# Kernel optimization log

Hardware: AMD Instinct MI355X
Metric: run time of the kernel (lower is better)

Reference implementation:

```python
import jax, jax.numpy as jnp
import numpy as np

N, E, T, H, D_IN, D_OUT = 50000, 320000, 4, 4, 128, 128
NEG_SLOPE = 0.2
LN_EPS = 1e-5


def setup_inputs() -> dict:
    key = jax.random.key(0)
    ks = jax.random.split(key, 10)
    x = jax.random.normal(ks[0], (N, D_IN), jnp.float32)
    edge_index = jax.random.randint(ks[1], (2, E), 0, N, jnp.int32)
    edge_attr = jax.random.randint(ks[2], (E,), 0, T, jnp.int32)
    W_gat = jax.random.normal(ks[3], (T, D_IN, H * D_OUT), jnp.float32) / np.sqrt(D_IN)
    a_src = jax.random.normal(ks[4], (T, H, D_OUT), jnp.float32) / np.sqrt(D_OUT)
    a_dst = jax.random.normal(ks[5], (T, H, D_OUT), jnp.float32) / np.sqrt(D_OUT)
    b_gat = jnp.zeros((T, D_OUT), jnp.float32)
    edge_type_weights = jnp.ones((T,), jnp.float32) / T
    W_fuse = jax.random.normal(ks[6], (T * D_OUT, D_OUT), jnp.float32) / np.sqrt(T * D_OUT)
    b_fuse = jnp.zeros((D_OUT,), jnp.float32)
    ln_gamma = jnp.ones((D_OUT,), jnp.float32)
    ln_beta = jnp.zeros((D_OUT,), jnp.float32)
    return {"x": x, "edge_index": edge_index, "edge_attr": edge_attr,
            "W_gat": W_gat, "a_src": a_src, "a_dst": a_dst, "b_gat": b_gat,
            "edge_type_weights": edge_type_weights, "W_fuse": W_fuse,
            "b_fuse": b_fuse, "ln_gamma": ln_gamma, "ln_beta": ln_beta}


def _gat_one_type(x, src_all, dst_all, mask_all, W, a_s, a_d, b):
    # x: [N, D_in]; src_all/dst_all: [E+N] (type-mask + self-loops on all nodes)
    n = x.shape[0]
    h = (x @ W).reshape(n, H, D_OUT)                      # [N, H, D]
    alpha_s = jnp.sum(h * a_s, axis=-1)                   # [N, H]
    alpha_d = jnp.sum(h * a_d, axis=-1)                   # [N, H]
    logit = jax.nn.leaky_relu(alpha_s[src_all] + alpha_d[dst_all], NEG_SLOPE)  # [Ea, H]
    neg_inf = jnp.float32(-1e30)
    logit = jnp.where(mask_all[:, None], logit, neg_inf)
    m = jax.ops.segment_max(logit, dst_all, num_segments=n)   # [N, H] (self-loops ensure finite)
    ex = jnp.exp(logit - m[dst_all])
    ex = jnp.where(mask_all[:, None], ex, 0.0)
    denom = jax.ops.segment_sum(ex, dst_all, num_segments=n)  # [N, H]
    alpha = ex / denom[dst_all]                                # [Ea, H]
    msg = alpha[:, :, None] * h[src_all]                       # [Ea, H, D]
    out = jax.ops.segment_sum(msg, dst_all, num_segments=n)   # [N, H, D]
    return out.mean(axis=1) + b                                # concat=False -> head mean


def reference(x, edge_index, edge_attr, W_gat, a_src, a_dst, b_gat,
              edge_type_weights, W_fuse, b_fuse, ln_gamma, ln_beta):
    n = x.shape[0]
    self_idx = jnp.arange(n, dtype=edge_index.dtype)
    src_all = jnp.concatenate([edge_index[0], self_idx])
    dst_all = jnp.concatenate([edge_index[1], self_idx])
    outs = []
    for t in range(T):
        mask_all = jnp.concatenate([edge_attr == t, jnp.ones((n,), bool)])
        outs.append(_gat_one_type(x, src_all, dst_all, mask_all,
                                  W_gat[t], a_src[t], a_dst[t], b_gat[t]))
    w = jax.nn.softmax(edge_type_weights)
    x_cat = jnp.concatenate([outs[t] * w[t] for t in range(T)], axis=1)  # [N, T*D]
    y = x_cat @ W_fuse + b_fuse
    mu = jnp.mean(y, axis=-1, keepdims=True)
    var = jnp.var(y, axis=-1, keepdims=True)
    y = (y - mu) / jnp.sqrt(var + LN_EPS) * ln_gamma + ln_beta
    return jax.nn.relu(y)
```

## Files before the change

### kernel.cpp

```cpp
#include <hip/hip_runtime.h>
#include <hip/hip_bf16.h>

#define TT 4
#define HH 4
#define DD 128
#define KAGG 2048

typedef __attribute__((ext_vector_type(8))) short short8;
typedef __attribute__((ext_vector_type(4))) float f32x4;

__device__ __forceinline__ float lrelu(float z) { return z > 0.f ? z : 0.2f * z; }
__device__ __forceinline__ float bf2f(unsigned short u) {
  union { unsigned int i; float f; } v; v.i = ((unsigned int)u) << 16; return v.f;
}
__device__ __forceinline__ unsigned short f2b(float f) {
  union { float f; unsigned int i; } u; u.f = f;
  unsigned int r = u.i + 0x7fff + ((u.i >> 16) & 1);
  return (unsigned short)(r >> 16);
}
__device__ __forceinline__ void unpack8(uint4 u, float* hv) {
  hv[0] = bf2f((unsigned short)(u.x & 0xffff));
  hv[1] = bf2f((unsigned short)(u.x >> 16));
  hv[2] = bf2f((unsigned short)(u.y & 0xffff));
  hv[3] = bf2f((unsigned short)(u.y >> 16));
  hv[4] = bf2f((unsigned short)(u.z & 0xffff));
  hv[5] = bf2f((unsigned short)(u.z >> 16));
  hv[6] = bf2f((unsigned short)(u.w & 0xffff));
  hv[7] = bf2f((unsigned short)(u.w >> 16));
}

__global__ __launch_bounds__(256) void convx_kernel(
    const float* __restrict__ x, unsigned short* __restrict__ xb, int total4) {
  int i = blockIdx.x * 256 + threadIdx.x;
  if (i >= total4) return;
  float4 v = ((const float4*)x)[i];
  ushort4 o;
  o.x = f2b(v.x); o.y = f2b(v.y); o.z = f2b(v.z); o.w = f2b(v.w);
  ((ushort4*)xb)[i] = o;
}

__global__ __launch_bounds__(256) void prepw_kernel(
    const float* __restrict__ Wg, const float* __restrict__ a_s,
    const float* __restrict__ a_d, const float* __restrict__ W_fuse,
    const float* __restrict__ b_gat, const float* __restrict__ etw,
    const float* __restrict__ b_fuse, unsigned short* __restrict__ Gfrag,
    unsigned short* __restrict__ Pall, float* __restrict__ cbias) {
  float e0 = etw[0], e1 = etw[1], e2 = etw[2], e3 = etw[3];
  float mx = fmaxf(fmaxf(e0, e1), fmaxf(e2, e3));
  float w0 = __expf(e0 - mx), w1 = __expf(e1 - mx), w2 = __expf(e2 - mx),
        w3 = __expf(e3 - mx);
  float inv = 1.f / (w0 + w1 + w2 + w3);
  float wts[4] = {w0 * inv, w1 * inv, w2 * inv, w3 * inv};

  int bid = blockIdx.x;
  if (bid < 1024) {
    int idx = bid * 256 + threadIdx.x;
    int f = idx >> 9, l = (idx >> 3) & 63, j = idx & 7;
    int kt = f >> 5, kk = (f >> 3) & 3, n = f & 7;
    int K = kt * 128 + kk * 32 + (l >> 4) * 8 + j;
    int col = n * 16 + (l & 15);
    int t = K >> 9, head = (K >> 7) & 3, k = K & 127;
    const float* wr = Wg + (size_t)t * 65536 + k * 512 + head * 128;
    const float* wf = W_fuse + (size_t)t * 128 * 128 + col;
    float s = 0.f;
    for (int m = 0; m < 128; ++m) s += wr[m] * wf[(size_t)m * 128];
    Gfrag[idx] = f2b(0.25f * wts[t] * s);
  } else if (bid < 1040) {
    int idx = (bid - 1024) * 256 + threadIdx.x;
    int c = idx >> 7, k = idx & 127;
    int t = c >> 3, jj = c & 7, head = jj & 3;
    const float* av = ((jj < 4) ? a_s : a_d) + (t * 4 + head) * 128;
    const float* wr = Wg + (size_t)t * 65536 + k * 512 + head * 128;
    float s = 0.f;
    for (int m = 0; m < 128; ++m) s += wr[m] * av[m];
    Pall[c * 128 + k] = f2b(s);
  } else {
    int j = threadIdx.x;
    if (j < 128) {
      float s = b_fuse[j];
      for (int t = 0; t < 4; ++t) {
        float st = 0.f;
        for (int m = 0; m < 128; ++m)
          st += b_gat[t * 128 + m] * W_fuse[(size_t)(t * 128 + m) * 128 + j];
        s += wts[t] * st;
      }
      cbias[j] = s;
    }
  }
}

__global__ __launch_bounds__(256) void alpha_mfma_kernel(
    const unsigned short* __restrict__ xb, const unsigned short* __restrict__ Pall,
    float* __restrict__ as_, float* __restrict__ ad_, int N) {
  __shared__ uint4 ldsv[2048];
  unsigned char* lds = (unsigned char*)ldsv;
  const int n0 = blockIdx.x * 128;
  const int tid = threadIdx.x, lane = tid & 63, wid = tid >> 6;
  const int lr = lane & 15, lg = lane >> 4;
#pragma unroll
  for (int i = 0; i < 8; ++i) {
    int chunk = tid + i * 256;
    int row = chunk >> 4, k16 = chunk & 15;
    int gr = n0 + row;
    uint4 v = make_uint4(0, 0, 0, 0);
    if (gr < N) v = *(const uint4*)(xb + (size_t)gr * DD + k16 * 8);
    *(uint4*)(lds + ((row * 256 + k16 * 16) ^ ((row & 7) << 4))) = v;
  }
  __syncthreads();
  f32x4 acc[2][2] = {};
#pragma unroll
  for (int kk = 0; kk < 4; ++kk) {
    short8 a[2], b[2];
#pragma unroll
    for (int m = 0; m < 2; ++m) {
      int row = wid * 32 + m * 16 + lr;
      a[m] = *(const short8*)(lds + ((row * 256 + kk * 64 + (lg << 4)) ^ ((row & 7) << 4)));
    }
#pragma unroll
    for (int n = 0; n < 2; ++n) {
      int c = n * 16 + lr;
      b[n] = *(const short8*)(Pall + c * DD + kk * 32 + lg * 8);
    }
#pragma unroll
    for (int m = 0; m < 2; ++m)
#pragma unroll
      for (int n = 0; n < 2; ++n)
        acc[m][n] = __builtin_amdgcn_mfma_f32_16x16x32_bf16(a[m], b[n], acc[m][n], 0, 0, 0);
  }
#pragma unroll
  for (int m = 0; m < 2; ++m)
#pragma unroll
    for (int n = 0; n < 2; ++n) {
      int c = n * 16 + lr;
      int t = c >> 3, jj = c & 7, head = jj & 3;
      float* dstp = (jj & 4) ? ad_ : as_;
#pragma unroll
      for (int r = 0; r < 4; ++r) {
        int gr = n0 + wid * 32 + m * 16 + lg * 4 + r;
        if (gr < N) dstp[((size_t)t * N + gr) * 4 + head] = acc[m][n][r];
      }
    }
}

__global__ __launch_bounds__(256) void hist_kernel(
    const int* __restrict__ dst, const int* __restrict__ attr,
    int* __restrict__ deg, int E, int N) {
  int e = blockIdx.x * 256 + threadIdx.x;
  if (e < E) atomicAdd(&deg[attr[e] * N + dst[e]], 1);
}

__global__ __launch_bounds__(1024) void scan1_kernel(
    const int* __restrict__ deg, int* __restrict__ rowptr,
    int* __restrict__ sums, int M) {
  __shared__ int sh[1024];
  int i = blockIdx.x * 1024 + threadIdx.x;
  int v = (i < M) ? deg[i] : 0;
  sh[threadIdx.x] = v;
  __syncthreads();
  for (int off = 1; off < 1024; off <<= 1) {
    int x = (threadIdx.x >= off) ? sh[threadIdx.x - off] : 0;
    __syncthreads();
    sh[threadIdx.x] += x;
    __syncthreads();
  }
  if (i < M) rowptr[i] = sh[threadIdx.x] - v;
  if (threadIdx.x == 1023) sums[blockIdx.x] = sh[1023];
}

__global__ __launch_bounds__(256) void scan2_kernel(int* __restrict__ sums, int nch) {
  __shared__ int sh[256];
  int v = (threadIdx.x < nch) ? sums[threadIdx.x] : 0;
  sh[threadIdx.x] = v;
  __syncthreads();
  for (int off = 1; off < 256; off <<= 1) {
    int x = (threadIdx.x >= off) ? sh[threadIdx.x - off] : 0;
    __syncthreads();
    sh[threadIdx.x] += x;
    __syncthreads();
  }
  if (threadIdx.x < nch) sums[threadIdx.x] = sh[threadIdx.x] - v;
}

__global__ __launch_bounds__(1024) void scan3_kernel(
    int* __restrict__ rowptr, const int* __restrict__ sums,
    int* __restrict__ cursor, int M) {
  int i = blockIdx.x * 1024 + threadIdx.x;
  if (i < M) {
    int r = rowptr[i] + sums[blockIdx.x];
    rowptr[i] = r;
    cursor[i] = r;
  }
}

__global__ __launch_bounds__(256) void scatter_kernel(
    const int* __restrict__ src, const int* __restrict__ dst,
    const int* __restrict__ attr, int* __restrict__ cursor,
    int* __restrict__ slist, int E, int N) {
  int e = blockIdx.x * 256 + threadIdx.x;
  if (e >= E) return;
  int p = atomicAdd(&cursor[attr[e] * N + dst[e]], 1);
  slist[p] = src[e];
}

__global__ __launch_bounds__(256) void gather_kernel(
    const int* __restrict__ slist, const int* __restrict__ rowptr,
    const int* __restrict__ deg, const float* __restrict__ as_,
    const float* __restrict__ ad_, const unsigned short* __restrict__ xb,
    unsigned short* __restrict__ AGG, int N) {
  int t = blockIdx.y;
  int d = blockIdx.x * 4 + (threadIdx.x >> 6);
  if (d >= N) return;
  int lane = threadIdx.x & 63;
  int head = lane >> 4;
  int dofs = (lane & 15) * 8;
  size_t tn = (size_t)t * N;

  float adh = ad_[(tn + d) * 4 + head];
  float es = __expf(lrelu(as_[(tn + d) * 4 + head] + adh));
  float den = es;
  float acc8[8], hv[8];
  unpack8(*(const uint4*)(xb + (size_t)d * DD + dofs), hv);
#pragma unroll
  for (int j = 0; j < 8; ++j) acc8[j] = es * hv[j];

  int base = rowptr[tn + d], dg = deg[tn + d];
  int i = 0;
  for (; i + 1 < dg; i += 2) {
    int s0 = slist[base + i], s1 = slist[base + i + 1];
    float av0 = as_[(tn + s0) * 4 + head];
    float av1 = as_[(tn + s1) * 4 + head];
    uint4 u0 = *(const uint4*)(xb + (size_t)s0 * DD + dofs);
    uint4 u1 = *(const uint4*)(xb + (size_t)s1 * DD + dofs);
    float q0 = __expf(lrelu(av0 + adh));
    float q1 = __expf(lrelu(av1 + adh));
    den += q0 + q1;
    unpack8(u0, hv);
#pragma unroll
    for (int j = 0; j < 8; ++j) acc8[j] += q0 * hv[j];
    unpack8(u1, hv);
#pragma unroll
    for (int j = 0; j < 8; ++j) acc8[j] += q1 * hv[j];
  }
  if (i < dg) {
    int s = slist[base + i];
    float av = as_[(tn + s) * 4 + head];
    uint4 u = *(const uint4*)(xb + (size_t)s * DD + dofs);
    float q = __expf(lrelu(av + adh));
    den += q;
    unpack8(u, hv);
#pragma unroll
    for (int j = 0; j < 8; ++j) acc8[j] += q * hv[j];
  }

  float r = 1.f / den;
  unsigned int p0 = (unsigned)f2b(acc8[0] * r) | ((unsigned)f2b(acc8[1] * r) << 16);
  unsigned int p1 = (unsigned)f2b(acc8[2] * r) | ((unsigned)f2b(acc8[3] * r) << 16);
  unsigned int p2 = (unsigned)f2b(acc8[4] * r) | ((unsigned)f2b(acc8[5] * r) << 16);
  unsigned int p3 = (unsigned)f2b(acc8[6] * r) | ((unsigned)f2b(acc8[7] * r) << 16);
  *(uint4*)(AGG + (size_t)d * KAGG + t * 512 + lane * 8) = make_uint4(p0, p1, p2, p3);
}

__global__ __launch_bounds__(256) void gemmln_kernel(
    const unsigned short* __restrict__ AGG, const unsigned short* __restrict__ Gfrag,
    const float* __restrict__ cbias, const float* __restrict__ gamma,
    const float* __restrict__ beta, float* __restrict__ out, int N) {
  __shared__ uint4 bbuf[2][2048];
  const int n0 = blockIdx.x * 128;
  const int tid = threadIdx.x, lane = tid & 63, wid = tid >> 6;
  const int lr = lane & 15, lg = lane >> 4;
  const int wrow = n0 + wid * 32;

  uint4 bn[8], an[8], ac[8];
#pragma unroll
  for (int i = 0; i < 8; ++i)
    bn[i] = *(const uint4*)(Gfrag + (size_t)(i * 256 + tid) * 8);
#pragma unroll
  for (int i = 0; i < 8; ++i) {
    int m = i >> 2, kk = i & 3;
    int gr = wrow + m * 16 + lr;
    an[i] = make_uint4(0, 0, 0, 0);
    if (gr < N) an[i] = *(const uint4*)(AGG + (size_t)gr * KAGG + kk * 32 + lg * 8);
  }
#pragma unroll
  for (int i = 0; i < 8; ++i) bbuf[0][i * 256 + tid] = bn[i];
  __syncthreads();
#pragma unroll
  for (int i = 0; i < 8; ++i) ac[i] = an[i];

  f32x4 acc[2][8] = {};
  int cur = 0;
  for (int kt = 0; kt < 16; ++kt) {
    if (kt < 15) {
#pragma unroll
      for (int i = 0; i < 8; ++i)
        bn[i] = *(const uint4*)(Gfrag + (size_t)(kt + 1) * 16384 + (size_t)(i * 256 + tid) * 8);
#pragma unroll
      for (int i = 0; i < 8; ++i) {
        int m = i >> 2, kk = i & 3;
        int gr = wrow + m * 16 + lr;
        an[i] = make_uint4(0, 0, 0, 0);
        if (gr < N)
          an[i] = *(const uint4*)(AGG + (size_t)gr * KAGG + (kt + 1) * 128 + kk * 32 + lg * 8);
      }
    }
    const unsigned char* lds = (const unsigned char*)bbuf[cur];
#pragma unroll
    for (int kk = 0; kk < 4; ++kk) {
      short8 a0 = *(const short8*)&ac[0 * 4 + kk];
      short8 a1 = *(const short8*)&ac[1 * 4 + kk];
#pragma unroll
      for (int n = 0; n < 8; ++n) {
        short8 b = *(const short8*)(lds + (kk * 8 + n) * 1024 + lane * 16);
        acc[0][n] = __builtin_amdgcn_mfma_f32_16x16x32_bf16(a0, b, acc[0][n], 0, 0, 0);
        acc[1][n] = __builtin_amdgcn_mfma_f32_16x16x32_bf16(a1, b, acc[1][n], 0, 0, 0);
      }
    }
    if (kt < 15) {
#pragma unroll
      for (int i = 0; i < 8; ++i) bbuf[cur ^ 1][i * 256 + tid] = bn[i];
      __syncthreads();
      cur ^= 1;
#pragma unroll
      for (int i = 0; i < 8; ++i) ac[i] = an[i];
    }
  }

  float cb[8], gm[8], bt[8];
#pragma unroll
  for (int n = 0; n < 8; ++n) {
    cb[n] = cbias[n * 16 + lr];
    gm[n] = gamma[n * 16 + lr];
    bt[n] = beta[n * 16 + lr];
  }
#pragma unroll
  for (int m = 0; m < 2; ++m)
#pragma unroll
    for (int rr = 0; rr < 4; ++rr) {
      float y[8];
      float s = 0.f, ss = 0.f;
#pragma unroll
      for (int n = 0; n < 8; ++n) {
        y[n] = acc[m][n][rr] + cb[n];
        s += y[n];
        ss += y[n] * y[n];
      }
#pragma unroll
      for (int mask = 1; mask <= 8; mask <<= 1) {
        s += __shfl_xor(s, mask);
        ss += __shfl_xor(ss, mask);
      }
      float mean = s * (1.f / 128.f);
      float var = ss * (1.f / 128.f) - mean * mean;
      float rstd = rsqrtf(var + 1e-5f);
      int gr = wrow + m * 16 + lg * 4 + rr;
      if (gr < N) {
#pragma unroll
        for (int n = 0; n < 8; ++n) {
          float v = (y[n] - mean) * rstd * gm[n] + bt[n];
          out[(size_t)gr * DD + n * 16 + lr] = fmaxf(0.f, v);
        }
      }
    }
}

extern "C" void kernel_launch(void* const* d_in, const int* in_sizes, int n_in,
                              void* d_out, int out_size, void* d_ws, size_t ws_size,
                              hipStream_t stream) {
  const float* x      = (const float*)d_in[0];
  const int*   ei     = (const int*)d_in[1];
  const int*   attr   = (const int*)d_in[2];
  const float* Wg     = (const float*)d_in[3];
  const float* a_src  = (const float*)d_in[4];
  const float* a_dst  = (const float*)d_in[5];
  const float* b_gat  = (const float*)d_in[6];
  const float* etw    = (const float*)d_in[7];
  const float* W_fuse = (const float*)d_in[8];
  const float* b_fuse = (const float*)d_in[9];
  const float* gamma  = (const float*)d_in[10];
  const float* beta   = (const float*)d_in[11];

  const int N = in_sizes[0] / DD;
  const int E = in_sizes[2];
  const int* src = ei;
  const int* dst = ei + E;
  const int M = TT * N;

  char* ws = (char*)d_ws;
  size_t off = 0;
  auto alloc = [&](size_t bytes) {
    void* p = ws + off;
    off += (bytes + 255) & ~(size_t)255;
    return p;
  };
  unsigned short* AGG   = (unsigned short*)alloc((size_t)N * KAGG * 2);
  unsigned short* xb    = (unsigned short*)alloc((size_t)N * DD * 2);
  unsigned short* Gfrag = (unsigned short*)alloc((size_t)512 * 512 * 2);
  unsigned short* Pall  = (unsigned short*)alloc((size_t)32 * DD * 2);
  float* cbias          = (float*)alloc(128 * sizeof(float));
  float* as_            = (float*)alloc((size_t)TT * N * 4 * sizeof(float));
  float* ad_            = (float*)alloc((size_t)TT * N * 4 * sizeof(float));
  int* deg              = (int*)alloc((size_t)M * sizeof(int));
  int* rowptr           = (int*)alloc((size_t)M * sizeof(int));
  int* cursor           = (int*)alloc((size_t)M * sizeof(int));
  int* slist            = (int*)alloc((size_t)E * sizeof(int));
  int* sums             = (int*)alloc(1024 * sizeof(int));

  hipMemsetAsync(deg, 0, (size_t)M * sizeof(int), stream);

  int total4x = N * DD / 4;
  convx_kernel<<<(total4x + 255) / 256, 256, 0, stream>>>(x, xb, total4x);
  prepw_kernel<<<1041, 256, 0, stream>>>(Wg, a_src, a_dst, W_fuse, b_gat, etw,
                                         b_fuse, Gfrag, Pall, cbias);
  hist_kernel<<<(E + 255) / 256, 256, 0, stream>>>(dst, attr, deg, E, N);
  int nch = (M + 1023) / 1024;
  scan1_kernel<<<nch, 1024, 0, stream>>>(deg, rowptr, sums, M);
  scan2_kernel<<<1, 256, 0, stream>>>(sums, nch);
  scan3_kernel<<<nch, 1024, 0, stream>>>(rowptr, sums, cursor, M);
  scatter_kernel<<<(E + 255) / 256, 256, 0, stream>>>(src, dst, attr, cursor, slist, E, N);

  alpha_mfma_kernel<<<(N + 127) / 128, 256, 0, stream>>>(xb, Pall, as_, ad_, N);

  dim3 ggrid((N + 3) / 4, TT);
  gather_kernel<<<ggrid, 256, 0, stream>>>(slist, rowptr, deg, as_, ad_, xb, AGG, N);

  gemmln_kernel<<<(N + 127) / 128, 256, 0, stream>>>(AGG, Gfrag, cbias, gamma, beta,
                                                     (float*)d_out, N);
}
```

Before: 209.9 us.

## Fuse prologue, scan and scatter/alpha kernels; shortcut empty rows; nontemporal AGG traffic

Merges the bf16 conversion, weight precompute and degree histogram into one launch. It replaces the three-pass scan with a single-pass scan that claims per-block bases through a global atomic counter, and fuses the CSR scatter with the alpha MFMA kernel. This cuts several launches and dependency gaps. The gather kernel now copies the node's own features directly when a (node, type) pair has no incoming edges, skipping the softmax work. AGG stores and loads use nontemporal hints to limit cache pollution. The atomic-based scan leaves segment order nondeterministic, but offsets stay disjoint.

```diff
diff --git a/kernel.cpp b/kernel.cpp
--- a/kernel.cpp
+++ b/kernel.cpp
@@ -8,6 +8,7 @@
 
 typedef __attribute__((ext_vector_type(8))) short short8;
 typedef __attribute__((ext_vector_type(4))) float f32x4;
+typedef __attribute__((ext_vector_type(4))) unsigned int uint4v;
 
 __device__ __forceinline__ float lrelu(float z) { return z > 0.f ? z : 0.2f * z; }
 __device__ __forceinline__ float bf2f(unsigned short u) {
@@ -18,7 +19,7 @@
   unsigned int r = u.i + 0x7fff + ((u.i >> 16) & 1);
   return (unsigned short)(r >> 16);
 }
-__device__ __forceinline__ void unpack8(uint4 u, float* hv) {
+__device__ __forceinline__ void unpack8v(uint4v u, float* hv) {
   hv[0] = bf2f((unsigned short)(u.x & 0xffff));
   hv[1] = bf2f((unsigned short)(u.x >> 16));
   hv[2] = bf2f((unsigned short)(u.y & 0xffff));
@@ -29,72 +30,120 @@
   hv[7] = bf2f((unsigned short)(u.w >> 16));
 }
 
-__global__ __launch_bounds__(256) void convx_kernel(
-    const float* __restrict__ x, unsigned short* __restrict__ xb, int total4) {
-  int i = blockIdx.x * 256 + threadIdx.x;
-  if (i >= total4) return;
-  float4 v = ((const float4*)x)[i];
-  ushort4 o;
-  o.x = f2b(v.x); o.y = f2b(v.y); o.z = f2b(v.z); o.w = f2b(v.w);
-  ((ushort4*)xb)[i] = o;
-}
-
-__global__ __launch_bounds__(256) void prepw_kernel(
+__global__ __launch_bounds__(256) void prologue_kernel(
+    const float* __restrict__ x, unsigned short* __restrict__ xb, int total4,
     const float* __restrict__ Wg, const float* __restrict__ a_s,
     const float* __restrict__ a_d, const float* __restrict__ W_fuse,
     const float* __restrict__ b_gat, const float* __restrict__ etw,
     const float* __restrict__ b_fuse, unsigned short* __restrict__ Gfrag,
-    unsigned short* __restrict__ Pall, float* __restrict__ cbias) {
-  float e0 = etw[0], e1 = etw[1], e2 = etw[2], e3 = etw[3];
-  float mx = fmaxf(fmaxf(e0, e1), fmaxf(e2, e3));
-  float w0 = __expf(e0 - mx), w1 = __expf(e1 - mx), w2 = __expf(e2 - mx),
-        w3 = __expf(e3 - mx);
-  float inv = 1.f / (w0 + w1 + w2 + w3);
-  float wts[4] = {w0 * inv, w1 * inv, w2 * inv, w3 * inv};
-
+    unsigned short* __restrict__ Pall, float* __restrict__ cbias,
+    const int* __restrict__ dst, const int* __restrict__ attr,
+    int* __restrict__ deg, int E, int N) {
   int bid = blockIdx.x;
-  if (bid < 1024) {
-    int idx = bid * 256 + threadIdx.x;
-    int f = idx >> 9, l = (idx >> 3) & 63, j = idx & 7;
-    int kt = f >> 5, kk = (f >> 3) & 3, n = f & 7;
-    int K = kt * 128 + kk * 32 + (l >> 4) * 8 + j;
-    int col = n * 16 + (l & 15);
-    int t = K >> 9, head = (K >> 7) & 3, k = K & 127;
-    const float* wr = Wg + (size_t)t * 65536 + k * 512 + head * 128;
-    const float* wf = W_fuse + (size_t)t * 128 * 128 + col;
-    float s = 0.f;
-    for (int m = 0; m < 128; ++m) s += wr[m] * wf[(size_t)m * 128];
-    Gfrag[idx] = f2b(0.25f * wts[t] * s);
-  } else if (bid < 1040) {
-    int idx = (bid - 1024) * 256 + threadIdx.x;
-    int c = idx >> 7, k = idx & 127;
-    int t = c >> 3, jj = c & 7, head = jj & 3;
-    const float* av = ((jj < 4) ? a_s : a_d) + (t * 4 + head) * 128;
-    const float* wr = Wg + (size_t)t * 65536 + k * 512 + head * 128;
-    float s = 0.f;
-    for (int m = 0; m < 128; ++m) s += wr[m] * av[m];
-    Pall[c * 128 + k] = f2b(s);
-  } else {
-    int j = threadIdx.x;
-    if (j < 128) {
-      float s = b_fuse[j];
-      for (int t = 0; t < 4; ++t) {
-        float st = 0.f;
-        for (int m = 0; m < 128; ++m)
-          st += b_gat[t * 128 + m] * W_fuse[(size_t)(t * 128 + m) * 128 + j];
-        s += wts[t] * st;
-      }
-      cbias[j] = s;
-    }
-  }
-}
-
-__global__ __launch_bounds__(256) void alpha_mfma_kernel(
-    const unsigned short* __restrict__ xb, const unsigned short* __restrict__ Pall,
-    float* __restrict__ as_, float* __restrict__ ad_, int N) {
+  const int nconv = (total4 + 255) >> 8;
+  if (bid < nconv) {
+    int i = bid * 256 + threadIdx.x;
+    if (i < total4) {
+      float4 v = ((const float4*)x)[i];
+      ushort4 o;
+      o.x = f2b(v.x); o.y = f2b(v.y); o.z = f2b(v.z); o.w = f2b(v.w);
+      ((ushort4*)xb)[i] = o;
+    }
+    return;
+  }
+  bid -= nconv;
+  if (bid < 1041) {
+    float e0 = etw[0], e1 = etw[1], e2 = etw[2], e3 = etw[3];
+    float mx = fmaxf(fmaxf(e0, e1), fmaxf(e2, e3));
+    float w0 = __expf(e0 - mx), w1 = __expf(e1 - mx), w2 = __expf(e2 - mx),
+          w3 = __expf(e3 - mx);
+    float inv = 1.f / (w0 + w1 + w2 + w3);
+    float wts[4] = {w0 * inv, w1 * inv, w2 * inv, w3 * inv};
+    if (bid < 1024) {
+      int idx = bid * 256 + threadIdx.x;
+      int f = idx >> 9, l = (idx >> 3) & 63, j = idx & 7;
+      int kt = f >> 5, kk = (f >> 3) & 3, n = f & 7;
+      int K = kt * 128 + kk * 32 + (l >> 4) * 8 + j;
+      int col = n * 16 + (l & 15);
+      int t = K >> 9, head = (K >> 7) & 3, k = K & 127;
+      const float* wr = Wg + (size_t)t * 65536 + k * 512 + head * 128;
+      const float* wf = W_fuse + (size_t)t * 128 * 128 + col;
+      float s = 0.f;
+      for (int m = 0; m < 128; ++m) s += wr[m] * wf[(size_t)m * 128];
+      Gfrag[idx] = f2b(0.25f * wts[t] * s);
+    } else if (bid < 1040) {
+      int idx = (bid - 1024) * 256 + threadIdx.x;
+      int c = idx >> 7, k = idx & 127;
+      int t = c >> 3, jj = c & 7, head = jj & 3;
+      const float* av = ((jj < 4) ? a_s : a_d) + (t * 4 + head) * 128;
+      const float* wr = Wg + (size_t)t * 65536 + k * 512 + head * 128;
+      float s = 0.f;
+      for (int m = 0; m < 128; ++m) s += wr[m] * av[m];
+      Pall[c * 128 + k] = f2b(s);
+    } else {
+      int j = threadIdx.x;
+      if (j < 128) {
+        float s = b_fuse[j];
+        for (int t = 0; t < 4; ++t) {
+          float st = 0.f;
+          for (int m = 0; m < 128; ++m)
+            st += b_gat[t * 128 + m] * W_fuse[(size_t)(t * 128 + m) * 128 + j];
+          s += wts[t] * st;
+        }
+        cbias[j] = s;
+      }
+    }
+    return;
+  }
+  bid -= 1041;
+  int e = bid * 256 + threadIdx.x;
+  if (e < E) atomicAdd(&deg[attr[e] * N + dst[e]], 1);
+}
+
+__global__ __launch_bounds__(1024) void scanfused_kernel(
+    const int* __restrict__ deg, int* __restrict__ rowptr,
+    int* __restrict__ cursor, int* __restrict__ gcur, int M) {
+  __shared__ int sh[1024];
+  __shared__ int base;
+  int i = blockIdx.x * 1024 + threadIdx.x;
+  int v = (i < M) ? deg[i] : 0;
+  sh[threadIdx.x] = v;
+  __syncthreads();
+  for (int off = 1; off < 1024; off <<= 1) {
+    int xx = (threadIdx.x >= off) ? sh[threadIdx.x - off] : 0;
+    __syncthreads();
+    sh[threadIdx.x] += xx;
+    __syncthreads();
+  }
+  if (threadIdx.x == 1023) base = atomicAdd(gcur, sh[1023]);
+  __syncthreads();
+  if (i < M) {
+    int r = base + sh[threadIdx.x] - v;
+    rowptr[i] = r;
+    cursor[i] = r;
+  }
+}
+
+__global__ __launch_bounds__(256) void scatter_alpha_kernel(
+    const int* __restrict__ src, const int* __restrict__ dst,
+    const int* __restrict__ attr, int* __restrict__ cursor,
+    int* __restrict__ slist, const unsigned short* __restrict__ xb,
+    const unsigned short* __restrict__ Pall, float* __restrict__ as_,
+    float* __restrict__ ad_, int E, int N) {
   __shared__ uint4 ldsv[2048];
+  int bid = blockIdx.x;
+  const int nsc = (E + 255) >> 8;
+  if (bid < nsc) {
+    int e = bid * 256 + threadIdx.x;
+    if (e < E) {
+      int p = atomicAdd(&cursor[attr[e] * N + dst[e]], 1);
+      slist[p] = src[e];
+    }
+    return;
+  }
+  bid -= nsc;
   unsigned char* lds = (unsigned char*)ldsv;
-  const int n0 = blockIdx.x * 128;
+  const int n0 = bid * 128;
   const int tid = threadIdx.x, lane = tid & 63, wid = tid >> 6;
   const int lr = lane & 15, lg = lane >> 4;
 #pragma unroll
@@ -140,66 +189,6 @@
         if (gr < N) dstp[((size_t)t * N + gr) * 4 + head] = acc[m][n][r];
       }
     }
-}
-
-__global__ __launch_bounds__(256) void hist_kernel(
-    const int* __restrict__ dst, const int* __restrict__ attr,
-    int* __restrict__ deg, int E, int N) {
-  int e = blockIdx.x * 256 + threadIdx.x;
-  if (e < E) atomicAdd(&deg[attr[e] * N + dst[e]], 1);
-}
-
-__global__ __launch_bounds__(1024) void scan1_kernel(
-    const int* __restrict__ deg, int* __restrict__ rowptr,
-    int* __restrict__ sums, int M) {
-  __shared__ int sh[1024];
-  int i = blockIdx.x * 1024 + threadIdx.x;
-  int v = (i < M) ? deg[i] : 0;
-  sh[threadIdx.x] = v;
-  __syncthreads();
-  for (int off = 1; off < 1024; off <<= 1) {
-    int x = (threadIdx.x >= off) ? sh[threadIdx.x - off] : 0;
-    __syncthreads();
-    sh[threadIdx.x] += x;
-    __syncthreads();
-  }
-  if (i < M) rowptr[i] = sh[threadIdx.x] - v;
-  if (threadIdx.x == 1023) sums[blockIdx.x] = sh[1023];
-}
-
-__global__ __launch_bounds__(256) void scan2_kernel(int* __restrict__ sums, int nch) {
-  __shared__ int sh[256];
-  int v = (threadIdx.x < nch) ? sums[threadIdx.x] : 0;
-  sh[threadIdx.x] = v;
-  __syncthreads();
-  for (int off = 1; off < 256; off <<= 1) {
-    int x = (threadIdx.x >= off) ? sh[threadIdx.x - off] : 0;
-    __syncthreads();
-    sh[threadIdx.x] += x;
-    __syncthreads();
-  }
-  if (threadIdx.x < nch) sums[threadIdx.x] = sh[threadIdx.x] - v;
-}
-
-__global__ __launch_bounds__(1024) void scan3_kernel(
-    int* __restrict__ rowptr, const int* __restrict__ sums,
-    int* __restrict__ cursor, int M) {
-  int i = blockIdx.x * 1024 + threadIdx.x;
-  if (i < M) {
-    int r = rowptr[i] + sums[blockIdx.x];
-    rowptr[i] = r;
-    cursor[i] = r;
-  }
-}
-
-__global__ __launch_bounds__(256) void scatter_kernel(
-    const int* __restrict__ src, const int* __restrict__ dst,
-    const int* __restrict__ attr, int* __restrict__ cursor,
-    int* __restrict__ slist, int E, int N) {
-  int e = blockIdx.x * 256 + threadIdx.x;
-  if (e >= E) return;
-  int p = atomicAdd(&cursor[attr[e] * N + dst[e]], 1);
-  slist[p] = src[e];
 }
 
 __global__ __launch_bounds__(256) void gather_kernel(
@@ -214,50 +203,58 @@
   int head = lane >> 4;
   int dofs = (lane & 15) * 8;
   size_t tn = (size_t)t * N;
+  uint4v* outp = (uint4v*)(AGG + (size_t)d * KAGG + t * 512 + lane * 8);
+
+  int base = rowptr[tn + d], dg = deg[tn + d];
+  if (dg == 0) {
+    uint4v u = *(const uint4v*)(xb + (size_t)d * DD + dofs);
+    __builtin_nontemporal_store(u, outp);
+    return;
+  }
 
   float adh = ad_[(tn + d) * 4 + head];
   float es = __expf(lrelu(as_[(tn + d) * 4 + head] + adh));
   float den = es;
   float acc8[8], hv[8];
-  unpack8(*(const uint4*)(xb + (size_t)d * DD + dofs), hv);
+  unpack8v(*(const uint4v*)(xb + (size_t)d * DD + dofs), hv);
 #pragma unroll
   for (int j = 0; j < 8; ++j) acc8[j] = es * hv[j];
 
-  int base = rowptr[tn + d], dg = deg[tn + d];
   int i = 0;
   for (; i + 1 < dg; i += 2) {
     int s0 = slist[base + i], s1 = slist[base + i + 1];
     float av0 = as_[(tn + s0) * 4 + head];
     float av1 = as_[(tn + s1) * 4 + head];
-    uint4 u0 = *(const uint4*)(xb + (size_t)s0 * DD + dofs);
-    uint4 u1 = *(const uint4*)(xb + (size_t)s1 * DD + dofs);
+    uint4v u0 = *(const uint4v*)(xb + (size_t)s0 * DD + dofs);
+    uint4v u1 = *(const uint4v*)(xb + (size_t)s1 * DD + dofs);
     float q0 = __expf(lrelu(av0 + adh));
     float q1 = __expf(lrelu(av1 + adh));
     den += q0 + q1;
-    unpack8(u0, hv);
+    unpack8v(u0, hv);
 #pragma unroll
     for (int j = 0; j < 8; ++j) acc8[j] += q0 * hv[j];
-    unpack8(u1, hv);
+    unpack8v(u1, hv);
 #pragma unroll
     for (int j = 0; j < 8; ++j) acc8[j] += q1 * hv[j];
   }
   if (i < dg) {
     int s = slist[base + i];
     float av = as_[(tn + s) * 4 + head];
-    uint4 u = *(const uint4*)(xb + (size_t)s * DD + dofs);
+    uint4v u = *(const uint4v*)(xb + (size_t)s * DD + dofs);
     float q = __expf(lrelu(av + adh));
     den += q;
-    unpack8(u, hv);
+    unpack8v(u, hv);
 #pragma unroll
     for (int j = 0; j < 8; ++j) acc8[j] += q * hv[j];
   }
 
   float r = 1.f / den;
-  unsigned int p0 = (unsigned)f2b(acc8[0] * r) | ((unsigned)f2b(acc8[1] * r) << 16);
-  unsigned int p1 = (unsigned)f2b(acc8[2] * r) | ((unsigned)f2b(acc8[3] * r) << 16);
-  unsigned int p2 = (unsigned)f2b(acc8[4] * r) | ((unsigned)f2b(acc8[5] * r) << 16);
-  unsigned int p3 = (unsigned)f2b(acc8[6] * r) | ((unsigned)f2b(acc8[7] * r) << 16);
-  *(uint4*)(AGG + (size_t)d * KAGG + t * 512 + lane * 8) = make_uint4(p0, p1, p2, p3);
+  uint4v o;
+  o.x = (unsigned)f2b(acc8[0] * r) | ((unsigned)f2b(acc8[1] * r) << 16);
+  o.y = (unsigned)f2b(acc8[2] * r) | ((unsigned)f2b(acc8[3] * r) << 16);
+  o.z = (unsigned)f2b(acc8[4] * r) | ((unsigned)f2b(acc8[5] * r) << 16);
+  o.w = (unsigned)f2b(acc8[6] * r) | ((unsigned)f2b(acc8[7] * r) << 16);
+  __builtin_nontemporal_store(o, outp);
 }
 
 __global__ __launch_bounds__(256) void gemmln_kernel(
@@ -270,7 +267,8 @@
   const int lr = lane & 15, lg = lane >> 4;
   const int wrow = n0 + wid * 32;
 
-  uint4 bn[8], an[8], ac[8];
+  uint4 bn[8], ac[8];
+  uint4v an[8];
 #pragma unroll
   for (int i = 0; i < 8; ++i)
     bn[i] = *(const uint4*)(Gfrag + (size_t)(i * 256 + tid) * 8);
@@ -278,14 +276,16 @@
   for (int i = 0; i < 8; ++i) {
     int m = i >> 2, kk = i & 3;
     int gr = wrow + m * 16 + lr;
-    an[i] = make_uint4(0, 0, 0, 0);
-    if (gr < N) an[i] = *(const uint4*)(AGG + (size_t)gr * KAGG + kk * 32 + lg * 8);
+    an[i] = (uint4v){0, 0, 0, 0};
+    if (gr < N)
+      an[i] = __builtin_nontemporal_load(
+          (const uint4v*)(AGG + (size_t)gr * KAGG + kk * 32 + lg * 8));
   }
 #pragma unroll
   for (int i = 0; i < 8; ++i) bbuf[0][i * 256 + tid] = bn[i];
   __syncthreads();
 #pragma unroll
-  for (int i = 0; i < 8; ++i) ac[i] = an[i];
+  for (int i = 0; i < 8; ++i) ac[i] = *(uint4*)&an[i];
 
   f32x4 acc[2][8] = {};
   int cur = 0;
@@ -298,9 +298,10 @@
       for (int i = 0; i < 8; ++i) {
         int m = i >> 2, kk = i & 3;
         int gr = wrow + m * 16 + lr;
-        an[i] = make_uint4(0, 0, 0, 0);
+        an[i] = (uint4v){0, 0, 0, 0};
         if (gr < N)
-          an[i] = *(const uint4*)(AGG + (size_t)gr * KAGG + (kt + 1) * 128 + kk * 32 + lg * 8);
+          an[i] = __builtin_nontemporal_load(
+              (const uint4v*)(AGG + (size_t)gr * KAGG + (kt + 1) * 128 + kk * 32 + lg * 8));
       }
     }
     const unsigned char* lds = (const unsigned char*)bbuf[cur];
@@ -321,7 +322,7 @@
       __syncthreads();
       cur ^= 1;
 #pragma unroll
-      for (int i = 0; i < 8; ++i) ac[i] = an[i];
+      for (int i = 0; i < 8; ++i) ac[i] = *(uint4*)&an[i];
     }
   }
 
@@ -399,26 +400,26 @@
   float* cbias          = (float*)alloc(128 * sizeof(float));
   float* as_            = (float*)alloc((size_t)TT * N * 4 * sizeof(float));
   float* ad_            = (float*)alloc((size_t)TT * N * 4 * sizeof(float));
-  int* deg              = (int*)alloc((size_t)M * sizeof(int));
+  int* deg              = (int*)alloc((size_t)(M + 1) * sizeof(int));
   int* rowptr           = (int*)alloc((size_t)M * sizeof(int));
   int* cursor           = (int*)alloc((size_t)M * sizeof(int));
   int* slist            = (int*)alloc((size_t)E * sizeof(int));
-  int* sums             = (int*)alloc(1024 * sizeof(int));
-
-  hipMemsetAsync(deg, 0, (size_t)M * sizeof(int), stream);
+
+  hipMemsetAsync(deg, 0, (size_t)(M + 1) * sizeof(int), stream);
 
   int total4x = N * DD / 4;
-  convx_kernel<<<(total4x + 255) / 256, 256, 0, stream>>>(x, xb, total4x);
-  prepw_kernel<<<1041, 256, 0, stream>>>(Wg, a_src, a_dst, W_fuse, b_gat, etw,
-                                         b_fuse, Gfrag, Pall, cbias);
-  hist_kernel<<<(E + 255) / 256, 256, 0, stream>>>(dst, attr, deg, E, N);
-  int nch = (M + 1023) / 1024;
-  scan1_kernel<<<nch, 1024, 0, stream>>>(deg, rowptr, sums, M);
-  scan2_kernel<<<1, 256, 0, stream>>>(sums, nch);
-  scan3_kernel<<<nch, 1024, 0, stream>>>(rowptr, sums, cursor, M);
-  scatter_kernel<<<(E + 255) / 256, 256, 0, stream>>>(src, dst, attr, cursor, slist, E, N);
-
-  alpha_mfma_kernel<<<(N + 127) / 128, 256, 0, stream>>>(xb, Pall, as_, ad_, N);
+  int nconv = (total4x + 255) / 256;
+  int nhist = (E + 255) / 256;
+  prologue_kernel<<<nconv + 1041 + nhist, 256, 0, stream>>>(
+      x, xb, total4x, Wg, a_src, a_dst, W_fuse, b_gat, etw, b_fuse,
+      Gfrag, Pall, cbias, dst, attr, deg, E, N);
+
+  scanfused_kernel<<<(M + 1023) / 1024, 1024, 0, stream>>>(deg, rowptr, cursor,
+                                                           deg + M, M);
+
+  int nalpha = (N + 127) / 128;
+  scatter_alpha_kernel<<<nhist + nalpha, 256, 0, stream>>>(
+      src, dst, attr, cursor, slist, xb, Pall, as_, ad_, E, N);
 
   dim3 ggrid((N + 3) / 4, TT);
   gather_kernel<<<ggrid, 256, 0, stream>>>(slist, rowptr, deg, as_, ad_, xb, AGG, N);
```

Measured after the change: 221.7 us. 5.6% more time.
